# Optimization experiments

Hardware: AMD Instinct MI355X
Metric: run time of the kernel (lower is better)

Reference implementation:

```python
import jax, jax.numpy as jnp
import numpy as np

DECAY = 0.5  # temporal_weight_decay


def setup_inputs() -> dict:
    key = jax.random.key(0)
    ks = jax.random.split(key, 8)
    B, N, D = 1, 128, 256
    T, Ncam, P, L = 4, 6, 17, 3
    WC = Ncam * P * L  # 306
    inp = {
        "content_queries": jax.random.normal(ks[0], (B, N, D), jnp.float32),
        "pixels": jax.random.uniform(ks[1], (B * T, N, Ncam, P, 2), jnp.float32),
        "ego_ts": jax.random.uniform(ks[2], (B, T), jnp.float32),
        "Ww": jax.random.normal(ks[3], (D, WC), jnp.float32) * (2.0 / (D + WC)) ** 0.5,
        "bw": jnp.zeros((WC,), jnp.float32),
        "feat_l0": jax.random.normal(ks[4], (Ncam, B * T, D, 64, 160), jnp.float32),
        "feat_l1": jax.random.normal(ks[5], (Ncam, B * T, D, 32, 80), jnp.float32),
        "feat_l2": jax.random.normal(ks[6], (Ncam, B * T, D, 16, 40), jnp.float32),
    }
    return inp


def _grid_sample(feat, gx, gy):
    """Bilinear grid_sample, align_corners=True, padding_mode='zeros'.
    feat: [Ncam, BT, C, H, W]; gx, gy: [BT, N, Ncam, P] in [-1, 1].
    Returns [BT, N, Ncam, P, C]."""
    Ncam, BT, C, H, W = feat.shape
    ix = (gx + 1.0) * 0.5 * (W - 1)
    iy = (gy + 1.0) * 0.5 * (H - 1)
    x0f = jnp.floor(ix)
    y0f = jnp.floor(iy)
    wx1 = ix - x0f
    wy1 = iy - y0f
    wx0 = 1.0 - wx1
    wy0 = 1.0 - wy1
    cam = jnp.arange(Ncam)[None, None, :, None]
    bt = jnp.arange(BT)[:, None, None, None]

    def gather(xf, yf):
        valid = (xf >= 0) & (xf <= W - 1) & (yf >= 0) & (yf <= H - 1)
        xc = jnp.clip(xf, 0, W - 1).astype(jnp.int32)
        yc = jnp.clip(yf, 0, H - 1).astype(jnp.int32)
        v = feat[cam, bt, :, yc, xc]  # [BT, N, Ncam, P, C]
        return v * valid[..., None].astype(feat.dtype)

    out = (gather(x0f, y0f) * (wx0 * wy0)[..., None]
           + gather(x0f + 1, y0f) * (wx1 * wy0)[..., None]
           + gather(x0f, y0f + 1) * (wx0 * wy1)[..., None]
           + gather(x0f + 1, y0f + 1) * (wx1 * wy1)[..., None])
    return out


def reference(content_queries, pixels, ego_ts, Ww, bw, feat_l0, feat_l1, feat_l2):
    B, N, D = content_queries.shape
    Ncam, BT, C, _, _ = feat_l0.shape
    T = BT // B
    P = pixels.shape[3]
    L = 3

    # per-query sigmoid weights over (cam, kpt, level)
    w = jax.nn.sigmoid(content_queries @ Ww + bw).reshape(B, N, Ncam, P, L)
    # temporal decay weights (no_grad in the original)
    td = ego_ts - ego_ts[:, -1:]
    tw = jax.lax.stop_gradient(jnp.exp(-jnp.square(td) / DECAY * 3.0))  # [B, T]
    w = w[:, None] * tw[:, :, None, None, None, None]  # [B,T,N,Ncam,P,L]
    w = w.reshape(BT, N, Ncam, P, L)
    invalid = pixels[..., 0] < 0.0  # [BT,N,Ncam,P]
    w = jnp.where(invalid[..., None], 0.0, w)
    # feature_dropout is identity in eval mode

    gx = pixels[..., 0] * 2.0 - 1.0
    gy = pixels[..., 1] * 2.0 - 1.0
    feats = jnp.stack([_grid_sample(f, gx, gy) for f in (feat_l0, feat_l1, feat_l2)],
                      axis=4)  # [BT, N, Ncam, P, L, C]

    fv = feats.reshape(B, T, N, Ncam, P, L, C)
    wv = w.reshape(B, T, N, Ncam, P, L)
    num = jnp.einsum('btncplf,btncpl->bnf', fv, wv)  # [B, N, C]
    den = jnp.clip(wv.sum(axis=(1, 3, 4, 5)), 1e-6, None)  # [B, N]
    agg = num / den[..., None]
    new_content_queries = jnp.concatenate([content_queries, agg], axis=-1)  # residual 'cat'
    return pixels, new_content_queries
```

## Files before the change

### kernel.cpp

```cpp
#include <hip/hip_runtime.h>

#define NQ   128
#define DIM  256
#define WCN  306
#define NCAM 6
#define PP   17
#define LV   3
#define TT   4
#define PIX_ELEMS 104448
#define OUT_CQ_OFF PIX_ELEMS
#define ROW  (2 * DIM)

#define SPAT_L0 245760
#define SPAT_L1 61440
#define SPAT_L2 15360
#define SPAT_TOTAL (SPAT_L0 + SPAT_L1 + SPAT_L2)
#define TF_ELEMS ((size_t)SPAT_TOTAL * 256)
#define TF_BYTES (TF_ELEMS * 2)
#define WB_BYTES ((size_t)NQ * WCN * 4)
#define DEN_BYTES ((size_t)NQ * 4)
#define WS_NEED  (TF_BYTES + WB_BYTES + DEN_BYTES)

#define SCH 12
#define RPB 102

typedef unsigned short u16;

__device__ __forceinline__ float b2f(u16 u) {
    union { unsigned int i; float f; } v;
    v.i = ((unsigned int)u) << 16;
    return v.f;
}
__device__ __forceinline__ u16 f2b(float f) {
    union { float f; unsigned int i; } v;
    v.f = f;
    unsigned int x = v.i;
    return (u16)((x + 0x7FFFu + ((x >> 16) & 1u)) >> 16);
}
__device__ __forceinline__ void calc_tw(const float* ego, float* tw) {
    float e3 = ego[TT - 1];
    #pragma unroll
    for (int t = 0; t < TT; ++t) {
        float d = ego[t] - e3;
        tw[t] = expf(-d * d * 6.0f);
    }
}

__global__ __launch_bounds__(320) void init_kernel(
    const float* __restrict__ cq, const float* __restrict__ Ww,
    const float* __restrict__ bw, const float* __restrict__ pixels,
    const float* __restrict__ ego,
    float* __restrict__ wbase, float* __restrict__ den,
    float* __restrict__ out)
{
    int bid = blockIdx.x, tid = threadIdx.x;
    if (bid < 128) {
        int n = bid;
        __shared__ float cqs[DIM];
        __shared__ float red[320];
        if (tid < DIM) cqs[tid] = cq[n * DIM + tid];
        __syncthreads();

        float denj = 0.f;
        if (tid < WCN) {
            int j = tid;
            float acc = bw[j];
            #pragma unroll 8
            for (int d = 0; d < DIM; ++d) acc += cqs[d] * Ww[d * WCN + j];
            float sig = 1.0f / (1.0f + expf(-acc));
            wbase[n * WCN + j] = sig;
            float tw[TT]; calc_tw(ego, tw);
            int cam = j / (PP * LV);
            int rem = j - cam * (PP * LV);
            int p   = rem / LV;
            float s = 0.f;
            #pragma unroll
            for (int t = 0; t < TT; ++t) {
                float px0 = pixels[(((t * NQ + n) * NCAM + cam) * PP + p) << 1];
                s += (px0 < 0.f) ? 0.f : tw[t];
            }
            denj = sig * s;
        }
        red[tid] = denj;
        __syncthreads();
        if (tid < 64) red[tid] += red[tid + 256];
        __syncthreads();
        for (int off = 128; off > 0; off >>= 1) {
            if (tid < off) red[tid] += red[tid + off];
            __syncthreads();
        }
        if (tid == 0) den[n] = fmaxf(red[0], 1e-6f);
    } else if (bid < 230) {
        if (tid < 256) {
            int v = (bid - 128) * 256 + tid;
            ((float4*)out)[v] = ((const float4*)pixels)[v];
        }
    } else {
        if (tid < 256) {
            int v = (bid - 230) * 256 + tid;
            int n  = v >> 6;
            int c4 = (v & 63) << 2;
            *(float4*)(out + OUT_CQ_OFF + n * ROW + DIM + c4) =
                make_float4(0.f, 0.f, 0.f, 0.f);
        }
    }
}

__global__ __launch_bounds__(256) void transpose_kernel(
    const float* __restrict__ f0, const float* __restrict__ f1,
    const float* __restrict__ f2, u16* __restrict__ tf)
{
    __shared__ float lds[64][65];
    int bid = blockIdx.x, tid = threadIdx.x;
    int plane, ctile, hwtile, HW, spat_base;
    const float* src;
    if (bid < 15360) {
        HW = 10240; src = f0; spat_base = 0;
        plane = bid / 640; int r = bid - plane * 640; ctile = r / 160; hwtile = r - ctile * 160;
    } else if (bid < 19200) {
        int b = bid - 15360; HW = 2560; src = f1; spat_base = SPAT_L0;
        plane = b / 160; int r = b - plane * 160; ctile = r / 40; hwtile = r - ctile * 40;
    } else {
        int b = bid - 19200; HW = 640; src = f2; spat_base = SPAT_L0 + SPAT_L1;
        plane = b / 40; int r = b - plane * 40; ctile = r / 10; hwtile = r - ctile * 10;
    }
    int hw0 = hwtile * 64;
    int c0  = ctile * 64;

    const float* sp = src + ((size_t)plane * 256 + c0) * HW + hw0;
    int cl = tid >> 4;
    int hl = (tid & 15) << 2;
    #pragma unroll
    for (int pass = 0; pass < 4; ++pass) {
        int c = pass * 16 + cl;
        float4 v = *(const float4*)(sp + (size_t)c * HW + hl);
        lds[hl + 0][c] = v.x; lds[hl + 1][c] = v.y;
        lds[hl + 2][c] = v.z; lds[hl + 3][c] = v.w;
    }
    __syncthreads();

    int hr = tid >> 4;
    int c4 = (tid & 15) << 2;
    u16* dp = tf + ((size_t)(spat_base + plane * HW + hw0)) * 256 + c0;
    #pragma unroll
    for (int pass = 0; pass < 4; ++pass) {
        int hw = pass * 16 + hr;
        ushort4 o = make_ushort4(f2b(lds[hw][c4 + 0]), f2b(lds[hw][c4 + 1]),
                                 f2b(lds[hw][c4 + 2]), f2b(lds[hw][c4 + 3]));
        *(ushort4*)(dp + (size_t)hw * 256 + c4) = o;
    }
}

__global__ __launch_bounds__(256) void gather_tr_kernel(
    const float* __restrict__ pixels, const float* __restrict__ ego,
    const float* __restrict__ wbase, const u16* __restrict__ tf,
    float* __restrict__ out)
{
    int bid = blockIdx.x;
    int n = bid / SCH;
    int chunk = bid - n * SCH;
    int tid = threadIdx.x;

    __shared__ int   offs[RPB][4];
    __shared__ float wts[RPB][4];
    __shared__ float red[4][DIM];

    if (tid < RPB) {
        int r = chunk * RPB + tid;
        int t = r / WCN;  int j = r - t * WCN;
        int cam = j / 51; int rem = j - cam * 51;
        int p = rem / 3;  int l = rem - p * 3;
        float e3 = ego[TT - 1];
        float dt = ego[t] - e3;
        float tw = expf(-dt * dt * 6.0f);
        int pidx = (((t * NQ + n) * NCAM + cam) * PP + p) << 1;
        float px0 = pixels[pidx], px1 = pixels[pidx + 1];
        float w = wbase[n * WCN + j] * tw;
        if (px0 < 0.f) w = 0.f;
        int W_ = (l == 0) ? 160 : ((l == 1) ? 80 : 40);
        int H_ = (l == 0) ? 64  : ((l == 1) ? 32 : 16);
        int HW = W_ * H_;
        int sb = (l == 0) ? 0 : ((l == 1) ? SPAT_L0 : (SPAT_L0 + SPAT_L1));
        float ix = px0 * (float)(W_ - 1);
        float iy = px1 * (float)(H_ - 1);
        float x0f = floorf(ix), y0f = floorf(iy);
        float wx1 = ix - x0f, wy1 = iy - y0f;
        float wx0 = 1.f - wx1, wy0 = 1.f - wy1;
        int x0 = (int)x0f, y0 = (int)y0f;
        int x1 = x0 + 1,  y1 = y0 + 1;
        bool vx0 = (x0 >= 0) & (x0 < W_), vx1 = (x1 >= 0) & (x1 < W_);
        bool vy0 = (y0 >= 0) & (y0 < H_), vy1 = (y1 >= 0) & (y1 < H_);
        int cx0 = min(max(x0, 0), W_ - 1), cx1 = min(max(x1, 0), W_ - 1);
        int cy0 = min(max(y0, 0), H_ - 1), cy1 = min(max(y1, 0), H_ - 1);
        int base = sb + (cam * TT + t) * HW;
        offs[tid][0] = base + cy0 * W_ + cx0;
        offs[tid][1] = base + cy0 * W_ + cx1;
        offs[tid][2] = base + cy1 * W_ + cx0;
        offs[tid][3] = base + cy1 * W_ + cx1;
        wts[tid][0] = w * wy0 * wx0 * ((vx0 & vy0) ? 1.f : 0.f);
        wts[tid][1] = w * wy0 * wx1 * ((vx1 & vy0) ? 1.f : 0.f);
        wts[tid][2] = w * wy1 * wx0 * ((vx0 & vy1) ? 1.f : 0.f);
        wts[tid][3] = w * wy1 * wx1 * ((vx1 & vy1) ? 1.f : 0.f);
    }
    __syncthreads();

    int wv   = tid >> 6;
    int lane = tid & 63;
    float acc0 = 0.f, acc1 = 0.f, acc2 = 0.f, acc3 = 0.f;

    const u16* tfl = tf + (lane << 2);

    int i = wv;
    float w0[4]; ushort4 v0[4];
    #pragma unroll
    for (int q = 0; q < 4; ++q) {
        w0[q] = wts[i][q];
        v0[q] = *(const ushort4*)(tfl + (size_t)offs[i][q] * 256);
    }
    while (true) {
        int inext = i + 4;
        bool have_next = (inext < RPB);
        float w1[4]; ushort4 v1[4];
        if (have_next) {
            #pragma unroll
            for (int q = 0; q < 4; ++q) {
                w1[q] = wts[inext][q];
                v1[q] = *(const ushort4*)(tfl + (size_t)offs[inext][q] * 256);
            }
        }
        #pragma unroll
        for (int q = 0; q < 4; ++q) {
            float wq = w0[q];
            acc0 += wq * b2f(v0[q].x);
            acc1 += wq * b2f(v0[q].y);
            acc2 += wq * b2f(v0[q].z);
            acc3 += wq * b2f(v0[q].w);
        }
        if (!have_next) break;
        i = inext;
        #pragma unroll
        for (int q = 0; q < 4; ++q) { w0[q] = w1[q]; v0[q] = v1[q]; }
    }

    int cb = lane << 2;
    red[wv][cb + 0] = acc0; red[wv][cb + 1] = acc1;
    red[wv][cb + 2] = acc2; red[wv][cb + 3] = acc3;
    __syncthreads();
    if (tid < DIM) {
        float s = red[0][tid] + red[1][tid] + red[2][tid] + red[3][tid];
        atomicAdd(&out[OUT_CQ_OFF + n * ROW + DIM + tid], s);
    }
}

__global__ __launch_bounds__(256) void epilogue_fast_kernel(
    const float* __restrict__ cq, const float* __restrict__ den,
    float* __restrict__ out)
{
    int n = blockIdx.x, tid = threadIdx.x;
    float d = den[n];
    float* row = out + OUT_CQ_OFF + n * ROW;
    row[tid] = cq[n * DIM + tid];
    row[DIM + tid] /= d;
}

__global__ __launch_bounds__(256) void copy_zero_kernel(
    const float* __restrict__ pixels, float* __restrict__ out)
{
    int bid = blockIdx.x, tid = threadIdx.x;
    if (bid < 102) {
        int v = bid * 256 + tid;
        ((float4*)out)[v] = ((const float4*)pixels)[v];
    } else {
        int v = (bid - 102) * 256 + tid;
        int n  = v >> 6;
        int c4 = (v & 63) << 2;
        float4* dst = (float4*)(out + OUT_CQ_OFF + n * ROW + DIM + c4);
        *dst = make_float4(0.f, 0.f, 0.f, 0.f);
    }
}

__global__ __launch_bounds__(256) void gather_kernel(
    const float* __restrict__ cq, const float* __restrict__ pixels,
    const float* __restrict__ ego, const float* __restrict__ Ww,
    const float* __restrict__ bw,
    const float* __restrict__ f0, const float* __restrict__ f1,
    const float* __restrict__ f2, float* __restrict__ out)
{
    int bid = blockIdx.x;
    int n   = bid & (NQ - 1);
    int g   = bid >> 7;
    int l   = g / NCAM;
    int cam = g - l * NCAM;
    int tid = threadIdx.x;

    __shared__ float cqs[DIM];
    __shared__ float ws[PP];
    __shared__ float pix[TT * PP * 2];
    __shared__ int4   offs4[TT * PP];
    __shared__ float4 wt4[TT * PP];

    cqs[tid] = cq[n * DIM + tid];
    if (tid < TT * PP * 2) {
        int t = tid / (PP * 2);
        int r = tid - t * (PP * 2);
        int p = r >> 1, comp = r & 1;
        pix[tid] = pixels[((((t * NQ + n) * NCAM + cam) * PP + p) << 1) + comp];
    }
    __syncthreads();

    if (tid < PP) {
        int j = cam * (PP * LV) + tid * LV + l;
        float acc = bw[j];
        #pragma unroll 8
        for (int d = 0; d < DIM; ++d) acc += cqs[d] * Ww[d * WCN + j];
        ws[tid] = 1.0f / (1.0f + expf(-acc));
    }
    __syncthreads();

    const int W_ = (l == 0) ? 160 : ((l == 1) ? 80 : 40);
    const int H_ = (l == 0) ? 64  : ((l == 1) ? 32 : 16);
    const int HW = W_ * H_;

    if (tid < TT * PP) {
        int t = tid / PP, p = tid - t * PP;
        float twl[TT]; calc_tw(ego, twl);
        float px0 = pix[(t * PP + p) * 2];
        float px1 = pix[(t * PP + p) * 2 + 1];
        float w = ws[p] * twl[t];
        if (px0 < 0.f) w = 0.f;
        float ix = px0 * (float)(W_ - 1);
        float iy = px1 * (float)(H_ - 1);
        float x0f = floorf(ix), y0f = floorf(iy);
        float wx1 = ix - x0f, wy1 = iy - y0f;
        float wx0 = 1.f - wx1, wy0 = 1.f - wy1;
        int x0 = (int)x0f, y0 = (int)y0f;
        int x1 = x0 + 1,  y1 = y0 + 1;
        bool vx0 = (x0 >= 0) & (x0 < W_), vx1 = (x1 >= 0) & (x1 < W_);
        bool vy0 = (y0 >= 0) & (y0 < H_), vy1 = (y1 >= 0) & (y1 < H_);
        int cx0 = min(max(x0, 0), W_ - 1), cx1 = min(max(x1, 0), W_ - 1);
        int cy0 = min(max(y0, 0), H_ - 1), cy1 = min(max(y1, 0), H_ - 1);
        offs4[tid] = make_int4(cy0 * W_ + cx0, cy0 * W_ + cx1,
                               cy1 * W_ + cx0, cy1 * W_ + cx1);
        wt4[tid] = make_float4(w * wy0 * wx0 * ((vx0 & vy0) ? 1.f : 0.f),
                               w * wy0 * wx1 * ((vx1 & vy0) ? 1.f : 0.f),
                               w * wy1 * wx0 * ((vx0 & vy1) ? 1.f : 0.f),
                               w * wy1 * wx1 * ((vx1 & vy1) ? 1.f : 0.f));
    }
    __syncthreads();

    const float* fbase = (l == 0) ? f0 : ((l == 1) ? f1 : f2);
    const float* base_c = fbase + (size_t)(cam * TT * DIM + tid) * (size_t)HW;

    float acc = 0.f;
    #pragma unroll
    for (int t = 0; t < TT; ++t) {
        const float* base = base_c + (size_t)t * (size_t)(DIM * HW);
        #pragma unroll 4
        for (int p = 0; p < PP; ++p) {
            int rr = t * PP + p;
            int4 o = offs4[rr];
            float4 w4 = wt4[rr];
            acc += w4.x * base[o.x] + w4.y * base[o.y]
                 + w4.z * base[o.z] + w4.w * base[o.w];
        }
    }
    atomicAdd(&out[OUT_CQ_OFF + n * ROW + DIM + tid], acc);
}

__global__ __launch_bounds__(512) void epilogue_kernel(
    const float* __restrict__ cq, const float* __restrict__ pixels,
    const float* __restrict__ ego, const float* __restrict__ Ww,
    const float* __restrict__ bw, float* __restrict__ out)
{
    int n = blockIdx.x, tid = threadIdx.x;
    __shared__ float cqs[DIM];
    __shared__ float red[512];
    __shared__ float dsh;

    if (tid < DIM) cqs[tid] = cq[n * DIM + tid];
    __syncthreads();

    float tw[TT]; calc_tw(ego, tw);

    float denj = 0.f;
    if (tid < WCN) {
        int j = tid;
        float acc = bw[j];
        #pragma unroll 8
        for (int d = 0; d < DIM; ++d) acc += cqs[d] * Ww[d * WCN + j];
        float sig = 1.0f / (1.0f + expf(-acc));
        int cam = j / (PP * LV);
        int rem = j - cam * (PP * LV);
        int p   = rem / LV;
        float s = 0.f;
        #pragma unroll
        for (int t = 0; t < TT; ++t) {
            float px0 = pixels[(((t * NQ + n) * NCAM + cam) * PP + p) << 1];
            s += (px0 < 0.f) ? 0.f : tw[t];
        }
        denj = sig * s;
    }
    red[tid] = denj;
    __syncthreads();
    for (int off = 256; off > 0; off >>= 1) {
        if (tid < off) red[tid] += red[tid + off];
        __syncthreads();
    }
    if (tid == 0) dsh = fmaxf(red[0], 1e-6f);
    __syncthreads();

    float den = dsh;
    float* row = out + OUT_CQ_OFF + n * ROW;
    if (tid < DIM) {
        row[tid] = cqs[tid];
        row[DIM + tid] /= den;
    }
}

extern "C" void kernel_launch(void* const* d_in, const int* in_sizes, int n_in,
                              void* d_out, int out_size, void* d_ws, size_t ws_size,
                              hipStream_t stream)
{
    const float* cq     = (const float*)d_in[0];
    const float* pixels = (const float*)d_in[1];
    const float* ego    = (const float*)d_in[2];
    const float* Ww     = (const float*)d_in[3];
    const float* bw     = (const float*)d_in[4];
    const float* f0     = (const float*)d_in[5];
    const float* f1     = (const float*)d_in[6];
    const float* f2     = (const float*)d_in[7];

    float* out = (float*)d_out;
    bool fast = (d_ws != nullptr) && (ws_size >= WS_NEED);

    if (fast) {
        u16*   tf    = (u16*)d_ws;
        float* wbase = (float*)((char*)d_ws + TF_BYTES);
        float* den   = (float*)((char*)d_ws + TF_BYTES + WB_BYTES);
        init_kernel<<<262, 320, 0, stream>>>(cq, Ww, bw, pixels, ego,
                                             wbase, den, out);
        transpose_kernel<<<20160, 256, 0, stream>>>(f0, f1, f2, tf);
        gather_tr_kernel<<<NQ * SCH, 256, 0, stream>>>(pixels, ego, wbase, tf, out);
        epilogue_fast_kernel<<<NQ, 256, 0, stream>>>(cq, den, out);
    } else {
        copy_zero_kernel<<<134, 256, 0, stream>>>(pixels, out);
        gather_kernel<<<18 * NQ, 256, 0, stream>>>(cq, pixels, ego, Ww, bw,
                                                   f0, f1, f2, out);
        epilogue_kernel<<<NQ, 512, 0, stream>>>(cq, pixels, ego, Ww, bw, out);
    }
}
```

Measured before the change: 474.5 us.

## Fuse init into transpose launch and pair adjacent-x taps into 16-byte gathers

Merges the weight/denominator init kernel and the bf16 transpose kernel into one launch with a uniform 256-thread block, removing one launch and the idle 320-thread tail. In the gather kernel, each pair of horizontally adjacent bilinear taps is fetched as a single 16-byte load: lanes in each half-wave cover the x0 and x0+1 pixels, which sit next to each other in the channel-last layout. This halves the number of offsets kept per row and doubles the bytes per load. It relies on the x0+1 pixel being stored right after x0. When x0 is clamped from a negative value, the x1 tap reads the wrong column, so correctness depends on in-range or masked pixels.

```diff
diff --git a/kernel.cpp b/kernel.cpp
--- a/kernel.cpp
+++ b/kernel.cpp
@@ -46,30 +46,33 @@
     }
 }
 
-__global__ __launch_bounds__(320) void init_kernel(
+__global__ __launch_bounds__(256) void prep_kernel(
     const float* __restrict__ cq, const float* __restrict__ Ww,
     const float* __restrict__ bw, const float* __restrict__ pixels,
     const float* __restrict__ ego,
+    const float* __restrict__ f0, const float* __restrict__ f1,
+    const float* __restrict__ f2,
     float* __restrict__ wbase, float* __restrict__ den,
-    float* __restrict__ out)
+    u16* __restrict__ tf, float* __restrict__ out)
 {
     int bid = blockIdx.x, tid = threadIdx.x;
+
     if (bid < 128) {
         int n = bid;
         __shared__ float cqs[DIM];
-        __shared__ float red[320];
-        if (tid < DIM) cqs[tid] = cq[n * DIM + tid];
+        __shared__ float redl[256];
+        cqs[tid] = cq[n * DIM + tid];
         __syncthreads();
 
+        float tw[TT]; calc_tw(ego, tw);
         float denj = 0.f;
-        if (tid < WCN) {
+        {
             int j = tid;
             float acc = bw[j];
             #pragma unroll 8
             for (int d = 0; d < DIM; ++d) acc += cqs[d] * Ww[d * WCN + j];
             float sig = 1.0f / (1.0f + expf(-acc));
             wbase[n * WCN + j] = sig;
-            float tw[TT]; calc_tw(ego, tw);
             int cam = j / (PP * LV);
             int rem = j - cam * (PP * LV);
             int p   = rem / LV;
@@ -81,48 +84,60 @@
             }
             denj = sig * s;
         }
-        red[tid] = denj;
-        __syncthreads();
-        if (tid < 64) red[tid] += red[tid + 256];
+        if (tid < WCN - 256) {
+            int j = tid + 256;
+            float acc = bw[j];
+            #pragma unroll 8
+            for (int d = 0; d < DIM; ++d) acc += cqs[d] * Ww[d * WCN + j];
+            float sig = 1.0f / (1.0f + expf(-acc));
+            wbase[n * WCN + j] = sig;
+            int cam = j / (PP * LV);
+            int rem = j - cam * (PP * LV);
+            int p   = rem / LV;
+            float s = 0.f;
+            #pragma unroll
+            for (int t = 0; t < TT; ++t) {
+                float px0 = pixels[(((t * NQ + n) * NCAM + cam) * PP + p) << 1];
+                s += (px0 < 0.f) ? 0.f : tw[t];
+            }
+            denj += sig * s;
+        }
+        redl[tid] = denj;
         __syncthreads();
         for (int off = 128; off > 0; off >>= 1) {
-            if (tid < off) red[tid] += red[tid + off];
+            if (tid < off) redl[tid] += redl[tid + off];
             __syncthreads();
         }
-        if (tid == 0) den[n] = fmaxf(red[0], 1e-6f);
-    } else if (bid < 230) {
-        if (tid < 256) {
-            int v = (bid - 128) * 256 + tid;
-            ((float4*)out)[v] = ((const float4*)pixels)[v];
-        }
-    } else {
-        if (tid < 256) {
-            int v = (bid - 230) * 256 + tid;
-            int n  = v >> 6;
-            int c4 = (v & 63) << 2;
-            *(float4*)(out + OUT_CQ_OFF + n * ROW + DIM + c4) =
-                make_float4(0.f, 0.f, 0.f, 0.f);
-        }
-    }
-}
-
-__global__ __launch_bounds__(256) void transpose_kernel(
-    const float* __restrict__ f0, const float* __restrict__ f1,
-    const float* __restrict__ f2, u16* __restrict__ tf)
-{
+        if (tid == 0) den[n] = fmaxf(redl[0], 1e-6f);
+        return;
+    }
+    if (bid < 230) {
+        int v = (bid - 128) * 256 + tid;
+        ((float4*)out)[v] = ((const float4*)pixels)[v];
+        return;
+    }
+    if (bid < 262) {
+        int v = (bid - 230) * 256 + tid;
+        int n  = v >> 6;
+        int c4 = (v & 63) << 2;
+        *(float4*)(out + OUT_CQ_OFF + n * ROW + DIM + c4) =
+            make_float4(0.f, 0.f, 0.f, 0.f);
+        return;
+    }
+
+    int b = bid - 262;
     __shared__ float lds[64][65];
-    int bid = blockIdx.x, tid = threadIdx.x;
     int plane, ctile, hwtile, HW, spat_base;
     const float* src;
-    if (bid < 15360) {
+    if (b < 15360) {
         HW = 10240; src = f0; spat_base = 0;
-        plane = bid / 640; int r = bid - plane * 640; ctile = r / 160; hwtile = r - ctile * 160;
-    } else if (bid < 19200) {
-        int b = bid - 15360; HW = 2560; src = f1; spat_base = SPAT_L0;
-        plane = b / 160; int r = b - plane * 160; ctile = r / 40; hwtile = r - ctile * 40;
+        plane = b / 640; int r = b - plane * 640; ctile = r / 160; hwtile = r - ctile * 160;
+    } else if (b < 19200) {
+        int b1 = b - 15360; HW = 2560; src = f1; spat_base = SPAT_L0;
+        plane = b1 / 160; int r = b1 - plane * 160; ctile = r / 40; hwtile = r - ctile * 40;
     } else {
-        int b = bid - 19200; HW = 640; src = f2; spat_base = SPAT_L0 + SPAT_L1;
-        plane = b / 40; int r = b - plane * 40; ctile = r / 10; hwtile = r - ctile * 10;
+        int b1 = b - 19200; HW = 640; src = f2; spat_base = SPAT_L0 + SPAT_L1;
+        plane = b1 / 40; int r = b1 - plane * 40; ctile = r / 10; hwtile = r - ctile * 10;
     }
     int hw0 = hwtile * 64;
     int c0  = ctile * 64;
@@ -161,9 +176,9 @@
     int chunk = bid - n * SCH;
     int tid = threadIdx.x;
 
-    __shared__ int   offs[RPB][4];
+    __shared__ int   offs[RPB][2];
     __shared__ float wts[RPB][4];
-    __shared__ float red[4][DIM];
+    __shared__ float red[8][DIM];
 
     if (tid < RPB) {
         int r = chunk * RPB + tid;
@@ -190,13 +205,11 @@
         int x1 = x0 + 1,  y1 = y0 + 1;
         bool vx0 = (x0 >= 0) & (x0 < W_), vx1 = (x1 >= 0) & (x1 < W_);
         bool vy0 = (y0 >= 0) & (y0 < H_), vy1 = (y1 >= 0) & (y1 < H_);
-        int cx0 = min(max(x0, 0), W_ - 1), cx1 = min(max(x1, 0), W_ - 1);
+        int cx0 = min(max(x0, 0), W_ - 1);
         int cy0 = min(max(y0, 0), H_ - 1), cy1 = min(max(y1, 0), H_ - 1);
         int base = sb + (cam * TT + t) * HW;
         offs[tid][0] = base + cy0 * W_ + cx0;
-        offs[tid][1] = base + cy0 * W_ + cx1;
-        offs[tid][2] = base + cy1 * W_ + cx0;
-        offs[tid][3] = base + cy1 * W_ + cx1;
+        offs[tid][1] = base + cy1 * W_ + cx0;
         wts[tid][0] = w * wy0 * wx0 * ((vx0 & vy0) ? 1.f : 0.f);
         wts[tid][1] = w * wy0 * wx1 * ((vx1 & vy0) ? 1.f : 0.f);
         wts[tid][2] = w * wy1 * wx0 * ((vx0 & vy1) ? 1.f : 0.f);
@@ -206,48 +219,52 @@
 
     int wv   = tid >> 6;
     int lane = tid & 63;
-    float acc0 = 0.f, acc1 = 0.f, acc2 = 0.f, acc3 = 0.f;
-
-    const u16* tfl = tf + (lane << 2);
+    int half = lane >> 5;
+    int lc   = lane & 31;
+    float acc[8];
+    #pragma unroll
+    for (int k = 0; k < 8; ++k) acc[k] = 0.f;
+
+    const u16* tfh = tf + half * 256 + lc * 8;
 
     int i = wv;
-    float w0[4]; ushort4 v0[4];
-    #pragma unroll
-    for (int q = 0; q < 4; ++q) {
-        w0[q] = wts[i][q];
-        v0[q] = *(const ushort4*)(tfl + (size_t)offs[i][q] * 256);
-    }
+    int   o0 = offs[i][0], o1 = offs[i][1];
+    float wA = wts[i][half], wB = wts[i][2 + half];
+    uint4 A = *(const uint4*)(tfh + (size_t)o0 * 256);
+    uint4 B = *(const uint4*)(tfh + (size_t)o1 * 256);
     while (true) {
         int inext = i + 4;
         bool have_next = (inext < RPB);
-        float w1[4]; ushort4 v1[4];
+        uint4 A1, B1; float wA1 = 0.f, wB1 = 0.f;
         if (have_next) {
-            #pragma unroll
-            for (int q = 0; q < 4; ++q) {
-                w1[q] = wts[inext][q];
-                v1[q] = *(const ushort4*)(tfl + (size_t)offs[inext][q] * 256);
-            }
-        }
+            int o0n = offs[inext][0], o1n = offs[inext][1];
+            wA1 = wts[inext][half]; wB1 = wts[inext][2 + half];
+            A1 = *(const uint4*)(tfh + (size_t)o0n * 256);
+            B1 = *(const uint4*)(tfh + (size_t)o1n * 256);
+        }
+        unsigned ua[4] = {A.x, A.y, A.z, A.w};
+        unsigned ub[4] = {B.x, B.y, B.z, B.w};
         #pragma unroll
-        for (int q = 0; q < 4; ++q) {
-            float wq = w0[q];
-            acc0 += wq * b2f(v0[q].x);
-            acc1 += wq * b2f(v0[q].y);
-            acc2 += wq * b2f(v0[q].z);
-            acc3 += wq * b2f(v0[q].w);
+        for (int k = 0; k < 4; ++k) {
+            acc[2 * k]     += wA * b2f((u16)(ua[k] & 0xFFFFu))
+                            + wB * b2f((u16)(ub[k] & 0xFFFFu));
+            acc[2 * k + 1] += wA * b2f((u16)(ua[k] >> 16))
+                            + wB * b2f((u16)(ub[k] >> 16));
         }
         if (!have_next) break;
         i = inext;
+        A = A1; B = B1; wA = wA1; wB = wB1;
+    }
+
+    int row = wv * 2 + half;
+    int cb = lc * 8;
+    #pragma unroll
+    for (int k = 0; k < 8; ++k) red[row][cb + k] = acc[k];
+    __syncthreads();
+    if (tid < DIM) {
+        float s = 0.f;
         #pragma unroll
-        for (int q = 0; q < 4; ++q) { w0[q] = w1[q]; v0[q] = v1[q]; }
-    }
-
-    int cb = lane << 2;
-    red[wv][cb + 0] = acc0; red[wv][cb + 1] = acc1;
-    red[wv][cb + 2] = acc2; red[wv][cb + 3] = acc3;
-    __syncthreads();
-    if (tid < DIM) {
-        float s = red[0][tid] + red[1][tid] + red[2][tid] + red[3][tid];
+        for (int r = 0; r < 8; ++r) s += red[r][tid];
         atomicAdd(&out[OUT_CQ_OFF + n * ROW + DIM + tid], s);
     }
 }
@@ -437,9 +454,8 @@
         u16*   tf    = (u16*)d_ws;
         float* wbase = (float*)((char*)d_ws + TF_BYTES);
         float* den   = (float*)((char*)d_ws + TF_BYTES + WB_BYTES);
-        init_kernel<<<262, 320, 0, stream>>>(cq, Ww, bw, pixels, ego,
-                                             wbase, den, out);
-        transpose_kernel<<<20160, 256, 0, stream>>>(f0, f1, f2, tf);
+        prep_kernel<<<20422, 256, 0, stream>>>(cq, Ww, bw, pixels, ego,
+                                               f0, f1, f2, wbase, den, tf, out);
         gather_tr_kernel<<<NQ * SCH, 256, 0, stream>>>(pixels, ego, wbase, tf, out);
         epilogue_fast_kernel<<<NQ, 256, 0, stream>>>(cq, den, out);
     } else {
```

After: 451.4 us. 4.9% less time.
